# Kernel tuning notes

Measured on AMD Instinct MI355X. Metric: run time of the kernel, lower is better.

Reference implementation:

```python
import jax, jax.numpy as jnp
import numpy as np

N, E, G, H = 50000, 800000, 2048, 128
DIS = 3  # dis_emb is None -> raw frac_diff (3 dims)
EIN = 2 * H + 6 + DIS  # 265


def _lin_init(key, fan_in, fan_out):
    lim = 1.0 / np.sqrt(fan_in)
    return jax.random.uniform(key, (fan_in, fan_out), jnp.float32, -lim, lim)


def setup_inputs() -> dict:
    key = jax.random.key(0)
    ks = jax.random.split(key, 12)
    node_features = jax.random.normal(ks[0], (N, H), jnp.float32)
    frac_coords = jax.random.uniform(ks[1], (N, 3), jnp.float32)
    lattices = jax.random.normal(ks[2], (G, 6), jnp.float32)
    frac_diff = jax.random.normal(ks[3], (E, 3), jnp.float32)
    edge_index = jax.random.randint(ks[4], (2, E), 0, N, jnp.int64 if jax.config.jax_enable_x64 else jnp.int32)
    edge2graph = jax.random.randint(ks[5], (E,), 0, G, edge_index.dtype)
    return dict(
        node_features=node_features,
        frac_coords=frac_coords,
        lattices=lattices,
        frac_diff=frac_diff,
        edge_index=edge_index,
        edge2graph=edge2graph,
        e_w1=_lin_init(ks[6], EIN, H), e_b1=jnp.zeros((H,), jnp.float32),
        e_w2=_lin_init(ks[7], H, H), e_b2=jnp.zeros((H,), jnp.float32),
        n_w1=_lin_init(ks[8], 2 * H, H), n_b1=jnp.zeros((H,), jnp.float32),
        n_w2=_lin_init(ks[9], H, H), n_b2=jnp.zeros((H,), jnp.float32),
    )


def reference(node_features, frac_coords, lattices, frac_diff, edge_index, edge2graph,
              e_w1, e_b1, e_w2, e_b2, n_w1, n_b1, n_w2, n_b2):
    n_nodes = node_features.shape[0]
    silu = jax.nn.silu
    # edge model: gather endpoints, concat with per-graph lattice + frac_diff
    hi = node_features[edge_index[0]]            # [E, H]
    hj = node_features[edge_index[1]]            # [E, H]
    lat = lattices[edge2graph]                   # [E, 6]
    edges_input = jnp.concatenate([hi, hj, lat, frac_diff], axis=1)  # [E, 265]
    e = silu(edges_input @ e_w1 + e_b1)
    edge_features = silu(e @ e_w2 + e_b2)        # [E, H]
    # scatter-mean aggregate onto source nodes
    seg = edge_index[0]
    agg_sum = jax.ops.segment_sum(edge_features, seg, num_segments=n_nodes)
    cnt = jax.ops.segment_sum(jnp.ones((edge_features.shape[0],), edge_features.dtype), seg, num_segments=n_nodes)
    agg = agg_sum / jnp.maximum(cnt, 1.0)[:, None]
    # node model + residual
    h = jnp.concatenate([node_features, agg], axis=1)  # [N, 2H]
    h = silu(h @ n_w1 + n_b1)
    node_output = silu(h @ n_w2 + n_b2)
    return node_features + node_output
```

## Files before the change

### kernel.cpp

```cpp
#include <hip/hip_runtime.h>

#define N_NODES 50000
#define N_EDGES 800000
#define HDIM 128
#define N_GRAPH 2048

typedef __bf16 bf16x8 __attribute__((ext_vector_type(8)));
typedef float f32x4 __attribute__((ext_vector_type(4)));

static __device__ __forceinline__ unsigned short f2bf(float f) {
    unsigned int u = __float_as_uint(f);
    u += 0x7fffu + ((u >> 16) & 1u);
    return (unsigned short)(u >> 16);
}
static __device__ __forceinline__ float bflo(unsigned int u) { return __uint_as_float(u << 16); }
static __device__ __forceinline__ float bfhi(unsigned int u) { return __uint_as_float(u & 0xFFFF0000u); }

static __device__ __forceinline__ unsigned int cvt_pk_bf16(float lo, float hi) {
    unsigned int r;
    asm("v_cvt_pk_bf16_f32 %0, %1, %2" : "=v"(r) : "v"(lo), "v"(hi));
    return r;
}

static __device__ __forceinline__ float silu_f(float x) {
    float e = __builtin_amdgcn_exp2f(x * -1.44269504f);
    return x * __builtin_amdgcn_rcpf(1.0f + e);
}

#define PREP_BLOCKS 1408
#define HIST_BLOCKS 3125
#define ZERO_BLOCKS 6250
__global__ void prep_hist_kernel(const float* __restrict__ ew1, const float* __restrict__ ew2,
                                 const float* __restrict__ nw1, const float* __restrict__ nw2,
                                 const float* __restrict__ eb1, const float* __restrict__ lattices,
                                 const int* __restrict__ eidx,
                                 unsigned short* __restrict__ W1aT, unsigned short* __restrict__ W1bT,
                                 unsigned short* __restrict__ W2t, unsigned short* __restrict__ N1t,
                                 unsigned short* __restrict__ N2t, unsigned short* __restrict__ Lb,
                                 int* __restrict__ buf, float* __restrict__ agg) {
    const int bid = blockIdx.x;
    if (bid >= PREP_BLOCKS + HIST_BLOCKS) {
        const int idx = (bid - PREP_BLOCKS - HIST_BLOCKS) * 256 + threadIdx.x;
        ((float4*)agg)[idx] = make_float4(0.f, 0.f, 0.f, 0.f);
        return;
    }
    if (bid >= PREP_BLOCKS) {
        int e = (bid - PREP_BLOCKS) * 256 + threadIdx.x;
        if (e < N_EDGES) atomicAdd(&buf[eidx[e]], 1);
        return;
    }
    int i = bid * 256 + threadIdx.x;
    if (i < 16384) {
        int n = i >> 7, k = i & 127;
        W1aT[i] = f2bf(ew1[k * 128 + n]);
    } else if (i < 32768) {
        int j = i - 16384; int n = j >> 7, k = j & 127;
        W1bT[j] = f2bf(ew1[(128 + k) * 128 + n]);
    } else if (i < 49152) {
        int j = i - 32768; int n = j >> 7, k = j & 127;
        W2t[j] = f2bf(ew2[k * 128 + n]);
    } else if (i < 81920) {
        int j = i - 49152; int n = j >> 8, k = j & 255;
        N1t[j] = f2bf(nw1[k * 128 + n]);
    } else if (i < 98304) {
        int j = i - 81920; int n = j >> 7, k = j & 127;
        N2t[j] = f2bf(nw2[k * 128 + n]);
    } else if (i < 98304 + 262144) {
        int j = i - 98304; int g = j >> 7, c = j & 127;
        float s = eb1[c];
#pragma unroll
        for (int t = 0; t < 6; ++t) s += lattices[g * 6 + t] * ew1[(256 + t) * 128 + c];
        Lb[j] = f2bf(s);
    }
}

__global__ __launch_bounds__(1024) void scan_kernel(int* __restrict__ buf) {
    constexpr int CH = 12288;
    __shared__ int lds[CH];
    __shared__ int part[1024];
    __shared__ int carry_s;
    const int t = threadIdx.x;
    if (t == 0) carry_s = 0;
    __syncthreads();
#pragma unroll 1
    for (int base = 0; base < N_NODES; base += CH) {
#pragma unroll
        for (int k = 0; k < CH / 1024; ++k) {
            int f = k * 1024 + t;
            lds[f] = (base + f < N_NODES) ? buf[base + f] : 0;
        }
        __syncthreads();
        int loc[12];
        int s = 0;
#pragma unroll
        for (int i = 0; i < 12; ++i) { loc[i] = lds[t * 12 + i]; s += loc[i]; }
        part[t] = s;
        __syncthreads();
        for (int off = 1; off < 1024; off <<= 1) {
            int tmp = (t >= off) ? part[t - off] : 0;
            __syncthreads();
            part[t] += tmp;
            __syncthreads();
        }
        const int total = part[1023];
        int run = carry_s + part[t] - s;
#pragma unroll
        for (int i = 0; i < 12; ++i) { int tmp = loc[i]; lds[t * 12 + i] = run; run += tmp; }
        __syncthreads();
#pragma unroll
        for (int k = 0; k < CH / 1024; ++k) {
            int f = k * 1024 + t;
            if (base + f < N_NODES) buf[base + f] = lds[f];
        }
        __syncthreads();
        if (t == 0) carry_s += total;
        __syncthreads();
    }
}

#define PERM_BLOCKS2 3125
#define PQ_BLOCKS ((N_NODES + 63) / 64)
__global__ __launch_bounds__(256, 4) void perm_pq_kernel(
    const int* __restrict__ eidx, const int* __restrict__ e2g,
    const float* __restrict__ frac_diff, int* __restrict__ buf,
    unsigned short* __restrict__ perm_lo, unsigned char* __restrict__ perm_hi,
    uint4* __restrict__ rec, const int packed,
    const float* __restrict__ nf, const unsigned short* __restrict__ W1aT,
    const unsigned short* __restrict__ W1bT,
    unsigned short* __restrict__ P, unsigned short* __restrict__ Qm) {
    constexpr int SA = 136;
    __shared__ unsigned short sm[64 * SA];
    const int bid = blockIdx.x;
    const int tid = threadIdx.x;

    if (bid < PERM_BLOCKS2) {
        int e = bid * 256 + tid;
        if (e < N_EDGES) {
            int s = eidx[e];
            int pos = atomicAdd(&buf[s], 1);
            if (packed) {
                int d = eidx[N_EDGES + e];
                int g = e2g[e];
                unsigned int w0 = (unsigned int)s | ((unsigned int)d << 16);
                unsigned int w1 = (unsigned int)g | ((unsigned int)f2bf(frac_diff[3 * e]) << 16);
                unsigned int w2 = (unsigned int)f2bf(frac_diff[3 * e + 1]) |
                                  ((unsigned int)f2bf(frac_diff[3 * e + 2]) << 16);
                rec[pos] = make_uint4(w0, w1, w2, 0u);
            } else {
                perm_lo[pos] = (unsigned short)(e & 0xFFFF);
                perm_hi[pos] = (unsigned char)(e >> 16);
            }
        }
        return;
    }

    const int n0 = (bid - PERM_BLOCKS2) * 64;
    const int mrow = tid >> 2, q = tid & 3;
    {
        const int node = n0 + mrow;
        unsigned short* row = sm + mrow * SA + q * 32;
        if (node < N_NODES) {
            const float4* a4 = (const float4*)(nf + (size_t)node * HDIM) + q * 8;
#pragma unroll
            for (int j = 0; j < 8; ++j) {
                float4 v = a4[j];
                *(ushort4*)(row + 4 * j) = make_ushort4(f2bf(v.x), f2bf(v.y), f2bf(v.z), f2bf(v.w));
            }
        } else {
#pragma unroll
            for (int j = 0; j < 8; ++j) *(ushort4*)(row + 4 * j) = make_ushort4(0, 0, 0, 0);
        }
    }
    __syncthreads();

    const int wave = tid >> 6, lane = tid & 63;
    const int lr = lane & 15, kq = lane >> 4;
    f32x4 acca[8] = {}, accb[8] = {};
    const int arow = (wave * 16 + lr) * SA;
#pragma unroll
    for (int ks = 0; ks < 128; ks += 32) {
        bf16x8 a = *(const bf16x8*)(sm + arow + ks + kq * 8);
#pragma unroll
        for (int nt = 0; nt < 8; ++nt) {
            bf16x8 ba = *(const bf16x8*)(W1aT + (nt * 16 + lr) * 128 + ks + kq * 8);
            acca[nt] = __builtin_amdgcn_mfma_f32_16x16x32_bf16(a, ba, acca[nt], 0, 0, 0);
            bf16x8 bb = *(const bf16x8*)(W1bT + (nt * 16 + lr) * 128 + ks + kq * 8);
            accb[nt] = __builtin_amdgcn_mfma_f32_16x16x32_bf16(a, bb, accb[nt], 0, 0, 0);
        }
    }
    __syncthreads();

    const int node = n0 + mrow;
#pragma unroll
    for (int nt = 0; nt < 8; ++nt) {
        const int col = nt * 16 + lr;
#pragma unroll
        for (int r = 0; r < 4; ++r)
            sm[(wave * 16 + kq * 4 + r) * SA + col] = f2bf(acca[nt][r]);
    }
    __syncthreads();
    if (node < N_NODES) {
        uint4* dst = (uint4*)(P + (size_t)node * HDIM + q * 32);
        const uint4* srcp = (const uint4*)(sm + mrow * SA + q * 32);
#pragma unroll
        for (int j = 0; j < 4; ++j) dst[j] = srcp[j];
    }
    __syncthreads();
#pragma unroll
    for (int nt = 0; nt < 8; ++nt) {
        const int col = nt * 16 + lr;
#pragma unroll
        for (int r = 0; r < 4; ++r)
            sm[(wave * 16 + kq * 4 + r) * SA + col] = f2bf(accb[nt][r]);
    }
    __syncthreads();
    if (node < N_NODES) {
        uint4* dst = (uint4*)(Qm + (size_t)node * HDIM + q * 32);
        const uint4* srcp = (const uint4*)(sm + mrow * SA + q * 32);
#pragma unroll
        for (int j = 0; j < 4; ++j) dst[j] = srcp[j];
    }
}

#define EDGE_NWG (N_EDGES / 64)
template <bool PACKED>
__global__ __launch_bounds__(256, 2) void edge_kernel(
    const unsigned short* __restrict__ P, const unsigned short* __restrict__ Qm,
    const unsigned short* __restrict__ Lb, const float* __restrict__ frac_diff,
    const int* __restrict__ eidx, const int* __restrict__ e2g,
    const unsigned short* __restrict__ perm_lo, const unsigned char* __restrict__ perm_hi,
    const uint4* __restrict__ rec,
    const float* __restrict__ e_w1, const unsigned short* __restrict__ W2t,
    const float* __restrict__ b2, float* __restrict__ agg) {
    const int tid = threadIdx.x;
    const int wv = tid >> 6, lane = tid & 63;
    const int lr = lane & 15, kq = lane >> 4;

    int bid = blockIdx.x;
    {
        constexpr int q = EDGE_NWG / 8, r = EDGE_NWG % 8;
        const int x = bid & 7, i = bid >> 3;
        bid = (x < r ? x * (q + 1) : r * (q + 1) + (x - r) * q) + i;
    }
    const int base = bid * 64 + wv * 16;

    int src, dst, g;
    float fd0, fd1, fd2;
    if (PACKED) {
        const uint4 rv = rec[base + lr];
        src = rv.x & 0xFFFF;
        dst = rv.x >> 16;
        g = rv.y & 0xFFFF;
        fd0 = bfhi(rv.y);
        fd1 = bflo(rv.z);
        fd2 = bfhi(rv.z);
    } else {
        const int i = base + lr;
        const int e = (int)perm_lo[i] | ((int)perm_hi[i] << 16);
        src = eidx[e];
        dst = eidx[N_EDGES + e];
        g = e2g[e];
        fd0 = frac_diff[3 * e];
        fd1 = frac_diff[3 * e + 1];
        fd2 = frac_diff[3 * e + 2];
    }

    int sc[4], sn[4];
#pragma unroll
    for (int r = 0; r < 4; ++r) {
        const int row = kq * 4 + r;
        sc[r] = __shfl(src, row);
        sn[r] = __shfl(src, (row + 1) & 15);
    }

    const float* wrbase = e_w1 + 262 * HDIM;
    bf16x8 afrag[4];
#pragma unroll
    for (int ks = 0; ks < 4; ++ks) {
        const int c0 = ks * 32 + kq * 8;
        uint4 pu = *(const uint4*)(P + (size_t)src * HDIM + c0);
        uint4 qu = *(const uint4*)(Qm + (size_t)dst * HDIM + c0);
        uint4 lu = *(const uint4*)(Lb + (size_t)g * HDIM + c0);
        float w0[8], w1[8], w2[8];
        *(float4*)(w0) = *(const float4*)(wrbase + c0);
        *(float4*)(w0 + 4) = *(const float4*)(wrbase + c0 + 4);
        *(float4*)(w1) = *(const float4*)(wrbase + 128 + c0);
        *(float4*)(w1 + 4) = *(const float4*)(wrbase + 128 + c0 + 4);
        *(float4*)(w2) = *(const float4*)(wrbase + 256 + c0);
        *(float4*)(w2 + 4) = *(const float4*)(wrbase + 256 + c0 + 4);
        const unsigned int* pw = (const unsigned int*)&pu;
        const unsigned int* qw = (const unsigned int*)&qu;
        const unsigned int* lw = (const unsigned int*)&lu;
        unsigned int ow[4];
#pragma unroll
        for (int w = 0; w < 4; ++w) {
            float x0 = bflo(pw[w]) + bflo(qw[w]) + bflo(lw[w])
                     + fd0 * w0[2 * w] + fd1 * w1[2 * w] + fd2 * w2[2 * w];
            float x1 = bfhi(pw[w]) + bfhi(qw[w]) + bfhi(lw[w])
                     + fd0 * w0[2 * w + 1] + fd1 * w1[2 * w + 1] + fd2 * w2[2 * w + 1];
            ow[w] = cvt_pk_bf16(silu_f(x0), silu_f(x1));
        }
        afrag[ks] = *(bf16x8*)ow;
    }

    f32x4 acc[8] = {};
#pragma unroll
    for (int ks = 0; ks < 4; ++ks) {
#pragma unroll
        for (int nt = 0; nt < 8; ++nt) {
            bf16x8 bb = *(const bf16x8*)(W2t + (nt * 16 + lr) * 128 + ks * 32 + kq * 8);
            acc[nt] = __builtin_amdgcn_mfma_f32_16x16x32_bf16(afrag[ks], bb, acc[nt], 0, 0, 0);
        }
    }

#pragma unroll
    for (int nt = 0; nt < 8; ++nt) {
        const int col = nt * 16 + lr;
        const float bias = b2[col];
        float p0 = silu_f(acc[nt][0] + bias);
        float p1 = p0 + silu_f(acc[nt][1] + bias);
        float p2 = p1 + silu_f(acc[nt][2] + bias);
        float p3 = p2 + silu_f(acc[nt][3] + bias);
        float t1 = __shfl_up(p3, 16);
        float t2 = __shfl_up(p3, 32);
        float t3 = __shfl_up(p3, 48);
        float off = 0.0f;
        if (kq > 0) off += t1;
        if (kq > 1) off += t2;
        if (kq > 2) off += t3;
        float pr[4] = { p0 + off, p1 + off, p2 + off, p3 + off };
#pragma unroll
        for (int r = 0; r < 4; ++r) {
            const int row = kq * 4 + r;
            const bool last = (row == 15);
            const bool bnd = last || (sc[r] != sn[r]);
            if (bnd) {
                atomicAdd(&agg[(size_t)sc[r] * HDIM + col], pr[r]);
                if (!last) atomicAdd(&agg[(size_t)sn[r] * HDIM + col], -pr[r]);
            }
        }
    }
}

__global__ __launch_bounds__(256, 4) void node_kernel(
    const float* __restrict__ nf, const float* __restrict__ agg,
    const int* __restrict__ buf,
    const unsigned short* __restrict__ N1t, const float* __restrict__ b1,
    const unsigned short* __restrict__ N2t, const float* __restrict__ b2,
    float* __restrict__ out) {
    constexpr int SA = 264;
    constexpr int S2 = 136;
    constexpr int SFo = 132;
    __shared__ unsigned short sm[64 * SA];
    float* smf = (float*)sm;

    const int tid = threadIdx.x;
    const int n0 = blockIdx.x * 64;
    const int mrow = tid >> 2, q = tid & 3;
    {
        const int node = n0 + mrow;
        unsigned short* row = sm + mrow * SA;
        const int cbq = q * 32;
        if (node < N_NODES) {
            const int c = buf[node] - (node ? buf[node - 1] : 0);
            const float inv = 1.0f / (float)max(c, 1);
            const float4* a4 = (const float4*)(nf + (size_t)node * HDIM) + q * 8;
            const float4* g4 = (const float4*)(agg + (size_t)node * HDIM) + q * 8;
#pragma unroll
            for (int j = 0; j < 8; ++j) {
                float4 v = a4[j];
                *(ushort4*)(row + cbq + 4 * j) =
                    make_ushort4(f2bf(v.x), f2bf(v.y), f2bf(v.z), f2bf(v.w));
                float4 g = g4[j];
                *(ushort4*)(row + HDIM + cbq + 4 * j) =
                    make_ushort4(f2bf(g.x * inv), f2bf(g.y * inv), f2bf(g.z * inv), f2bf(g.w * inv));
            }
        } else {
#pragma unroll
            for (int j = 0; j < 8; ++j) {
                *(ushort4*)(row + cbq + 4 * j) = make_ushort4(0, 0, 0, 0);
                *(ushort4*)(row + HDIM + cbq + 4 * j) = make_ushort4(0, 0, 0, 0);
            }
        }
    }
    __syncthreads();

    const int wave = tid >> 6, lane = tid & 63;
    const int lr = lane & 15, kq = lane >> 4;

    f32x4 acc[8] = {};
    const int arow = (wave * 16 + lr) * SA;
#pragma unroll
    for (int ks = 0; ks < 256; ks += 32) {
        bf16x8 a = *(const bf16x8*)(sm + arow + ks + kq * 8);
#pragma unroll
        for (int nt = 0; nt < 8; ++nt) {
            bf16x8 bb = *(const bf16x8*)(N1t + (nt * 16 + lr) * 256 + ks + kq * 8);
            acc[nt] = __builtin_amdgcn_mfma_f32_16x16x32_bf16(a, bb, acc[nt], 0, 0, 0);
        }
    }
    __syncthreads();

#pragma unroll
    for (int nt = 0; nt < 8; ++nt) {
        const int col = nt * 16 + lr;
        const float bias = b1[col];
#pragma unroll
        for (int r = 0; r < 4; ++r) {
            const int mm = wave * 16 + kq * 4 + r;
            sm[mm * S2 + col] = f2bf(silu_f(acc[nt][r] + bias));
        }
    }
    __syncthreads();

    f32x4 acc2[8] = {};
    const int arow2 = (wave * 16 + lr) * S2;
#pragma unroll
    for (int ks = 0; ks < 128; ks += 32) {
        bf16x8 a = *(const bf16x8*)(sm + arow2 + ks + kq * 8);
#pragma unroll
        for (int nt = 0; nt < 8; ++nt) {
            bf16x8 bb = *(const bf16x8*)(N2t + (nt * 16 + lr) * 128 + ks + kq * 8);
            acc2[nt] = __builtin_amdgcn_mfma_f32_16x16x32_bf16(a, bb, acc2[nt], 0, 0, 0);
        }
    }
    __syncthreads();

#pragma unroll
    for (int nt = 0; nt < 8; ++nt) {
        const int col = nt * 16 + lr;
        const float bias = b2[col];
#pragma unroll
        for (int r = 0; r < 4; ++r) {
            const int mm = wave * 16 + kq * 4 + r;
            smf[mm * SFo + col] = silu_f(acc2[nt][r] + bias);
        }
    }
    __syncthreads();
    {
        const int node = n0 + mrow;
        if (node < N_NODES) {
            const float4* nfr = (const float4*)(nf + (size_t)node * HDIM) + q * 8;
            float4* outr = (float4*)(out + (size_t)node * HDIM) + q * 8;
            const float* st = smf + mrow * SFo + q * 32;
#pragma unroll
            for (int j = 0; j < 8; ++j) {
                float4 v = nfr[j];
                float4 s4 = *(const float4*)(st + 4 * j);
                v.x += s4.x; v.y += s4.y; v.z += s4.z; v.w += s4.w;
                outr[j] = v;
            }
        }
    }
}

extern "C" void kernel_launch(void* const* d_in, const int* in_sizes, int n_in,
                              void* d_out, int out_size, void* d_ws, size_t ws_size,
                              hipStream_t stream) {
    const float* node_features = (const float*)d_in[0];
    const float* lattices = (const float*)d_in[2];
    const float* frac_diff = (const float*)d_in[3];
    const int* edge_index = (const int*)d_in[4];
    const int* edge2graph = (const int*)d_in[5];
    const float* e_w1 = (const float*)d_in[6];
    const float* e_b1 = (const float*)d_in[7];
    const float* e_w2 = (const float*)d_in[8];
    const float* e_b2 = (const float*)d_in[9];
    const float* n_w1 = (const float*)d_in[10];
    const float* n_b1 = (const float*)d_in[11];
    const float* n_w2 = (const float*)d_in[12];
    const float* n_b2 = (const float*)d_in[13];

    char* ws = (char*)d_ws;
    unsigned short* W1aT = (unsigned short*)(ws);
    unsigned short* W1bT = (unsigned short*)(ws + 32768);
    unsigned short* W2t  = (unsigned short*)(ws + 65536);
    unsigned short* N1t  = (unsigned short*)(ws + 98304);
    unsigned short* N2t  = (unsigned short*)(ws + 163840);
    unsigned short* Lb   = (unsigned short*)(ws + 196608);
    unsigned short* P    = (unsigned short*)(ws + 720896);
    unsigned short* Qm   = (unsigned short*)(ws + 13520896);
    int* buf             = (int*)(ws + 26320896);
    unsigned short* perm_lo = (unsigned short*)(ws + 26520896);
    unsigned char* perm_hi  = (unsigned char*)(ws + 28120896);
    uint4* rec           = (uint4*)(ws + 28920896);
    float* agg = (float*)d_out;

    const int packed = (ws_size >= 28920896 + (size_t)N_EDGES * 16) ? 1 : 0;

    hipMemsetAsync(buf, 0, (size_t)N_NODES * 4, stream);

    prep_hist_kernel<<<PREP_BLOCKS + HIST_BLOCKS + ZERO_BLOCKS, 256, 0, stream>>>(
        e_w1, e_w2, n_w1, n_w2, e_b1, lattices, edge_index,
        W1aT, W1bT, W2t, N1t, N2t, Lb, buf, agg);

    scan_kernel<<<1, 1024, 0, stream>>>(buf);

    perm_pq_kernel<<<PERM_BLOCKS2 + PQ_BLOCKS, 256, 0, stream>>>(
        edge_index, edge2graph, frac_diff, buf, perm_lo, perm_hi, rec, packed,
        node_features, W1aT, W1bT, P, Qm);

    if (packed) {
        edge_kernel<true><<<EDGE_NWG, 256, 0, stream>>>(
            P, Qm, Lb, frac_diff, edge_index, edge2graph, perm_lo, perm_hi, rec,
            e_w1, W2t, e_b2, agg);
    } else {
        edge_kernel<false><<<EDGE_NWG, 256, 0, stream>>>(
            P, Qm, Lb, frac_diff, edge_index, edge2graph, perm_lo, perm_hi, rec,
            e_w1, W2t, e_b2, agg);
    }

    node_kernel<<<(N_NODES + 63) / 64, 256, 0, stream>>>(
        node_features, agg, buf, N1t, n_b1, N2t, n_b2, (float*)d_out);
}
```

Measured before the change: 589.2 us.

## Switch edge MLP second layer to 32x32x16 MFMA with 32-edge wave tiles

```diff
diff --git a/kernel.cpp b/kernel.cpp
--- a/kernel.cpp
+++ b/kernel.cpp
@@ -7,6 +7,7 @@
 
 typedef __bf16 bf16x8 __attribute__((ext_vector_type(8)));
 typedef float f32x4 __attribute__((ext_vector_type(4)));
+typedef float f32x16 __attribute__((ext_vector_type(16)));
 
 static __device__ __forceinline__ unsigned short f2bf(float f) {
     unsigned int u = __float_as_uint(f);
@@ -222,9 +223,9 @@
     }
 }
 
-#define EDGE_NWG (N_EDGES / 64)
+#define EDGE_NWG (N_EDGES / 128)
 template <bool PACKED>
-__global__ __launch_bounds__(256, 2) void edge_kernel(
+__global__ __launch_bounds__(256, 3) void edge_kernel(
     const unsigned short* __restrict__ P, const unsigned short* __restrict__ Qm,
     const unsigned short* __restrict__ Lb, const float* __restrict__ frac_diff,
     const int* __restrict__ eidx, const int* __restrict__ e2g,
@@ -234,20 +235,13 @@
     const float* __restrict__ b2, float* __restrict__ agg) {
     const int tid = threadIdx.x;
     const int wv = tid >> 6, lane = tid & 63;
-    const int lr = lane & 15, kq = lane >> 4;
-
-    int bid = blockIdx.x;
-    {
-        constexpr int q = EDGE_NWG / 8, r = EDGE_NWG % 8;
-        const int x = bid & 7, i = bid >> 3;
-        bid = (x < r ? x * (q + 1) : r * (q + 1) + (x - r) * q) + i;
-    }
-    const int base = bid * 64 + wv * 16;
+    const int row = lane & 31, hi = lane >> 5;
+    const int base = blockIdx.x * 128 + wv * 32;
 
     int src, dst, g;
     float fd0, fd1, fd2;
     if (PACKED) {
-        const uint4 rv = rec[base + lr];
+        const uint4 rv = rec[base + row];
         src = rv.x & 0xFFFF;
         dst = rv.x >> 16;
         g = rv.y & 0xFFFF;
@@ -255,7 +249,7 @@
         fd1 = bflo(rv.z);
         fd2 = bfhi(rv.z);
     } else {
-        const int i = base + lr;
+        const int i = base + row;
         const int e = (int)perm_lo[i] | ((int)perm_hi[i] << 16);
         src = eidx[e];
         dst = eidx[N_EDGES + e];
@@ -265,22 +259,31 @@
         fd2 = frac_diff[3 * e + 2];
     }
 
-    int sc[4], sn[4];
-#pragma unroll
-    for (int r = 0; r < 4; ++r) {
-        const int row = kq * 4 + r;
-        sc[r] = __shfl(src, row);
-        sn[r] = __shfl(src, (row + 1) & 15);
-    }
+    const size_t prow = (size_t)src * HDIM;
+    const size_t qrow = (size_t)dst * HDIM;
+    const size_t lrow = (size_t)g * HDIM;
+    uint4 pu[8], qu[8], lu[8];
+#pragma unroll
+    for (int kk = 0; kk < 8; ++kk) {
+        const int c0 = kk * 16 + hi * 8;
+        pu[kk] = *(const uint4*)(P + prow + c0);
+        qu[kk] = *(const uint4*)(Qm + qrow + c0);
+        lu[kk] = *(const uint4*)(Lb + lrow + c0);
+    }
+
+    int sc[16], snq[4];
+#pragma unroll
+    for (int r = 0; r < 16; ++r)
+        sc[r] = __shfl(src, (r & 3) + 8 * (r >> 2) + 4 * hi);
+#pragma unroll
+    for (int j = 0; j < 4; ++j)
+        snq[j] = __shfl(src, (4 * (2 * j + hi) + 4) & 31);
 
     const float* wrbase = e_w1 + 262 * HDIM;
-    bf16x8 afrag[4];
-#pragma unroll
-    for (int ks = 0; ks < 4; ++ks) {
-        const int c0 = ks * 32 + kq * 8;
-        uint4 pu = *(const uint4*)(P + (size_t)src * HDIM + c0);
-        uint4 qu = *(const uint4*)(Qm + (size_t)dst * HDIM + c0);
-        uint4 lu = *(const uint4*)(Lb + (size_t)g * HDIM + c0);
+    bf16x8 afrag[8];
+#pragma unroll
+    for (int kk = 0; kk < 8; ++kk) {
+        const int c0 = kk * 16 + hi * 8;
         float w0[8], w1[8], w2[8];
         *(float4*)(w0) = *(const float4*)(wrbase + c0);
         *(float4*)(w0 + 4) = *(const float4*)(wrbase + c0 + 4);
@@ -288,9 +291,9 @@
         *(float4*)(w1 + 4) = *(const float4*)(wrbase + 128 + c0 + 4);
         *(float4*)(w2) = *(const float4*)(wrbase + 256 + c0);
         *(float4*)(w2 + 4) = *(const float4*)(wrbase + 256 + c0 + 4);
-        const unsigned int* pw = (const unsigned int*)&pu;
-        const unsigned int* qw = (const unsigned int*)&qu;
-        const unsigned int* lw = (const unsigned int*)&lu;
+        const unsigned int* pw = (const unsigned int*)&pu[kk];
+        const unsigned int* qw = (const unsigned int*)&qu[kk];
+        const unsigned int* lw = (const unsigned int*)&lu[kk];
         unsigned int ow[4];
 #pragma unroll
         for (int w = 0; w < 4; ++w) {
@@ -300,43 +303,54 @@
                      + fd0 * w0[2 * w + 1] + fd1 * w1[2 * w + 1] + fd2 * w2[2 * w + 1];
             ow[w] = cvt_pk_bf16(silu_f(x0), silu_f(x1));
         }
-        afrag[ks] = *(bf16x8*)ow;
-    }
-
-    f32x4 acc[8] = {};
-#pragma unroll
-    for (int ks = 0; ks < 4; ++ks) {
-#pragma unroll
-        for (int nt = 0; nt < 8; ++nt) {
-            bf16x8 bb = *(const bf16x8*)(W2t + (nt * 16 + lr) * 128 + ks * 32 + kq * 8);
-            acc[nt] = __builtin_amdgcn_mfma_f32_16x16x32_bf16(afrag[ks], bb, acc[nt], 0, 0, 0);
-        }
-    }
-
-#pragma unroll
-    for (int nt = 0; nt < 8; ++nt) {
-        const int col = nt * 16 + lr;
+        afrag[kk] = *(bf16x8*)ow;
+    }
+
+    f32x16 acc[4] = {};
+#pragma unroll
+    for (int kk = 0; kk < 8; ++kk) {
+#pragma unroll
+        for (int t4 = 0; t4 < 4; ++t4) {
+            bf16x8 bb = *(const bf16x8*)(W2t + (t4 * 32 + row) * 128 + kk * 16 + hi * 8);
+            acc[t4] = __builtin_amdgcn_mfma_f32_32x32x16_bf16(afrag[kk], bb, acc[t4], 0, 0, 0);
+        }
+    }
+
+#pragma unroll
+    for (int t4 = 0; t4 < 4; ++t4) {
+        const int col = t4 * 32 + row;
         const float bias = b2[col];
-        float p0 = silu_f(acc[nt][0] + bias);
-        float p1 = p0 + silu_f(acc[nt][1] + bias);
-        float p2 = p1 + silu_f(acc[nt][2] + bias);
-        float p3 = p2 + silu_f(acc[nt][3] + bias);
-        float t1 = __shfl_up(p3, 16);
-        float t2 = __shfl_up(p3, 32);
-        float t3 = __shfl_up(p3, 48);
-        float off = 0.0f;
-        if (kq > 0) off += t1;
-        if (kq > 1) off += t2;
-        if (kq > 2) off += t3;
-        float pr[4] = { p0 + off, p1 + off, p2 + off, p3 + off };
-#pragma unroll
-        for (int r = 0; r < 4; ++r) {
-            const int row = kq * 4 + r;
-            const bool last = (row == 15);
-            const bool bnd = last || (sc[r] != sn[r]);
-            if (bnd) {
-                atomicAdd(&agg[(size_t)sc[r] * HDIM + col], pr[r]);
-                if (!last) atomicAdd(&agg[(size_t)sn[r] * HDIM + col], -pr[r]);
+        float p[16], tq[4], to[4];
+#pragma unroll
+        for (int rq = 0; rq < 4; ++rq) {
+            float s0 = silu_f(acc[t4][4 * rq + 0] + bias);
+            float s1 = silu_f(acc[t4][4 * rq + 1] + bias);
+            float s2 = silu_f(acc[t4][4 * rq + 2] + bias);
+            float s3 = silu_f(acc[t4][4 * rq + 3] + bias);
+            p[4 * rq + 0] = s0;
+            p[4 * rq + 1] = s0 + s1;
+            p[4 * rq + 2] = p[4 * rq + 1] + s2;
+            p[4 * rq + 3] = p[4 * rq + 2] + s3;
+            tq[rq] = p[4 * rq + 3];
+            to[rq] = __shfl_xor(tq[rq], 32);
+        }
+        float cum = 0.f;
+#pragma unroll
+        for (int rq = 0; rq < 4; ++rq) {
+            const float off = cum + (hi ? to[rq] : 0.f);
+            cum += tq[rq] + to[rq];
+#pragma unroll
+            for (int i = 0; i < 4; ++i) {
+                const int r = 4 * rq + i;
+                const float val = p[r] + off;
+                const int myrow = 4 * (2 * rq + hi) + i;
+                const bool lastg = (myrow == 31);
+                const int nxt = (i < 3) ? sc[r + 1] : snq[rq];
+                const bool bnd = lastg || (sc[r] != nxt);
+                if (bnd) {
+                    atomicAdd(&agg[(size_t)sc[r] * HDIM + col], val);
+                    if (!lastg) atomicAdd(&agg[(size_t)nxt * HDIM + col], -val);
+                }
             }
         }
     }
```

Measured after the change: 544.4 us. 7.6% less time.
